# Kernel tuning notes

Measured on AMD Instinct MI355X. Metric: run time of the kernel, lower is better.

The kernel has to match this reference:

```python
import jax, jax.numpy as jnp
import numpy as np

L0, L1, L2 = 32, 16, 8
NS, NB = 512, 256
CUT = 7.0
N, E, G = 16384, 131072, 16
FEAT = L0 + 3 * L1 + 5 * L2  # 120


def setup_inputs() -> dict:
    key = jax.random.key(0)
    ks = jax.random.split(key, 16)
    rn = lambda k, s, sc=1.0: jax.random.normal(k, s, jnp.float32) * sc
    inp = {}
    inp['nodes'] = rn(ks[0], (N, FEAT))
    inp['pos'] = rn(ks[1], (N, 3)) * 5.0
    inp['cell'] = rn(ks[2], (G, 3, 3))
    inp['edge_shift'] = rn(ks[3], (E, 3))
    # tensor-product path weights (e3nn FullyConnectedTensorProduct, uvw mode)
    inp['W0'] = rn(ks[4], (L0, L0, NS))
    inp['W1'] = rn(ks[5], (L1, L1, NS))
    inp['W2'] = rn(ks[6], (L2, L2, NS))
    inp['ln_g'] = jnp.ones((NS,), jnp.float32)
    inp['ln_b'] = jnp.zeros((NS,), jnp.float32)
    inp['df_w1'] = rn(ks[7], (NB, 1024), NB ** -0.5)
    inp['df_b1'] = jnp.zeros((1024,), jnp.float32)
    inp['df_w2'] = rn(ks[8], (1024, NS), 1024 ** -0.5)
    inp['df_b2'] = jnp.zeros((NS,), jnp.float32)
    inp['mi_w1'] = rn(ks[9], (NS, 1024), NS ** -0.5)
    inp['mi_b1'] = jnp.zeros((1024,), jnp.float32)
    inp['mi_w2'] = rn(ks[10], (1024, 1024), 1024 ** -0.5)
    inp['mi_b2'] = jnp.zeros((1024,), jnp.float32)
    inp['mo_w'] = rn(ks[11], (1024, 1), 1024 ** -0.5)
    inp['mo_b'] = jnp.zeros((1,), jnp.float32)
    inp['edge_index'] = jax.random.randint(ks[12], (2, E), 0, N)
    inp['batch_vec'] = jnp.sort(jax.random.randint(ks[13], (N,), 0, G))
    return inp


def _split_irreps(x):
    x0 = x[:, :L0]                                   # (E, L0) scalars 0e
    x1 = x[:, L0:L0 + 3 * L1].reshape(-1, L1, 3)      # (E, L1, 3) vectors 1o
    x2 = x[:, L0 + 3 * L1:].reshape(-1, L2, 5)        # (E, L2, 5) 2e
    return x0, x1, x2


def reference(nodes, pos, cell, edge_shift, W0, W1, W2, ln_g, ln_b,
              df_w1, df_b1, df_w2, df_b2, mi_w1, mi_b1, mi_w2, mi_b2,
              mo_w, mo_b, edge_index, batch_vec):
    src, dst = edge_index[0], edge_index[1]
    # periodic-image translation vector per edge
    bcell = cell[batch_vec[src]]                      # (E,3,3)
    tvec = jnp.einsum('ei,eij->ej', edge_shift, bcell)
    radvec = pos[dst] - pos[src] + tvec               # (E,3)
    dist = jnp.linalg.norm(radvec, axis=1, keepdims=True)  # (E,1)
    r = 1.0 / (dist + 1e-6)
    # Bessel radial embedding with cutoff CUT, NB basis functions
    n = jnp.arange(1, NB + 1, dtype=jnp.float32)
    emb = jnp.sqrt(2.0 / CUT) * jnp.sin(n * jnp.pi * r / CUT) / r  # (E,NB)
    distfilter = jax.nn.silu(emb @ df_w1 + df_b1) @ df_w2 + df_b2  # (E,NS)

    # symmetrized fully-connected tensor product -> 0e scalars
    # 0.5*(tp(xs,xd)+tp(xd,xs)) == contraction of euv with symmetrized W
    xs0, xs1, xs2 = _split_irreps(nodes[src])
    xd0, xd1, xd2 = _split_irreps(nodes[dst])
    fan = jnp.sqrt(jnp.float32(L0 * L0 + L1 * L1 + L2 * L2))  # element path norm
    sym = lambda W: 0.5 * (W + W.transpose(1, 0, 2))
    e0 = jnp.einsum('eu,ev->euv', xs0, xd0)
    mixed = jnp.einsum('euv,uvw->ew', e0, sym(W0)) / fan
    e1 = jnp.einsum('eui,evi->euv', xs1, xd1)
    mixed = mixed + jnp.einsum('euv,uvw->ew', e1, sym(W1)) / (fan * jnp.sqrt(3.0))
    e2 = jnp.einsum('eui,evi->euv', xs2, xd2)
    mixed = mixed + jnp.einsum('euv,uvw->ew', e2, sym(W2)) / (fan * jnp.sqrt(5.0))

    # LayerNorm over numscalars
    mu = jnp.mean(mixed, axis=-1, keepdims=True)
    var = jnp.mean((mixed - mu) ** 2, axis=-1, keepdims=True)
    mixednorm = (mixed - mu) * jax.lax.rsqrt(var + 1e-5) * ln_g + ln_b

    reg = mixednorm * distfilter
    h = jax.nn.silu(reg @ mi_w1 + mi_b1)
    h = jax.nn.silu(h @ mi_w2 + mi_b2)
    return h @ mo_w + mo_b  # (E,1)
```

## Files before the change

### kernel.cpp

```cpp
#include <hip/hip_runtime.h>

#define EE 131072
#define NNODE 16384
#define FEAT 120
#define NS 512
#define NB 256
#define KCAT 1344

typedef unsigned short u16;
typedef __bf16 bf16x8 __attribute__((ext_vector_type(8)));
typedef float f32x4 __attribute__((ext_vector_type(4)));
typedef float f32x16 __attribute__((ext_vector_type(16)));
typedef unsigned short ushort8 __attribute__((ext_vector_type(8)));

__device__ __forceinline__ float b2f(u16 u) {
  union { unsigned int i; float f; } x; x.i = ((unsigned int)u) << 16; return x.f;
}
__device__ __forceinline__ u16 f2b(float f) {
  union { float f; unsigned int i; } x; x.f = f;
  unsigned int lsb = (x.i >> 16) & 1u;
  x.i += 0x7fffu + lsb;
  return (u16)(x.i >> 16);
}
__device__ __forceinline__ u16 f2b_fast(float f) {
  __bf16 h = (__bf16)f;
  union { __bf16 h; u16 u; } x; x.h = h; return x.u;
}
__device__ __forceinline__ float rdany(const void* p, long i, int f32) {
  return f32 ? ((const float*)p)[i] : b2f(((const u16*)p)[i]);
}

__device__ __forceinline__ void gload16(const u16* g, u16* l) {
  __builtin_amdgcn_global_load_lds(
      (__attribute__((address_space(1))) void*)(u16*)g,
      (__attribute__((address_space(3))) void*)l, 16, 0, 0);
}

__global__ void detect_k(const u16* __restrict__ nodes, int* __restrict__ flag) {
  __shared__ int cnt;
  if (threadIdx.x == 0) cnt = 0;
  __syncthreads();
  u16 v = nodes[threadIdx.x];
  int e = (v >> 7) & 0xFF;
  if (e >= 0x48) atomicAdd(&cnt, 1);
  __syncthreads();
  if (threadIdx.x == 0) *flag = (cnt >= 16) ? 1 : 0;
}

__global__ __launch_bounds__(256) void convert_k(const void* __restrict__ src,
                                                 u16* __restrict__ dst, long n,
                                                 const int* __restrict__ flag) {
  long i = (long)blockIdx.x * 256 + threadIdx.x;
  if (i >= n) return;
  if (*flag)
    dst[i] = f2b(((const float*)src)[i]);
  else
    dst[i] = ((const u16*)src)[i];
}

__global__ __launch_bounds__(256) void transpose_k(const u16* __restrict__ in,
                                                   u16* __restrict__ out, int R, int C) {
  __shared__ u16 tile[32][33];
  int c0 = blockIdx.x * 32, r0 = blockIdx.y * 32;
  int tx = threadIdx.x & 31, ty = threadIdx.x >> 5;
  for (int i = 0; i < 32; i += 8) {
    int r = r0 + ty + i, c = c0 + tx;
    if (r < R && c < C) tile[ty + i][tx] = in[(long)r * C + c];
  }
  __syncthreads();
  for (int i = 0; i < 32; i += 8) {
    int r = r0 + tx, c = c0 + ty + i;
    if (r < R && c < C) out[(long)c * R + r] = tile[tx][ty + i];
  }
}

__global__ __launch_bounds__(256) void build_wcat(const u16* __restrict__ W0,
                                                  const u16* __restrict__ W1,
                                                  const u16* __restrict__ W2,
                                                  u16* __restrict__ wcT) {
  int idx = blockIdx.x * 256 + threadIdx.x;
  if (idx >= NS * KCAT) return;
  int w = idx / KCAT, k = idx - w * KCAT;
  const float fan = 36.66060556f;
  float val;
  if (k < 1024) {
    int u = k >> 5, v = k & 31;
    val = 0.5f * (b2f(W0[(u * 32 + v) * NS + w]) + b2f(W0[(v * 32 + u) * NS + w])) / fan;
  } else if (k < 1280) {
    int j = k - 1024;
    int u = j >> 4, v = j & 15;
    val = 0.5f * (b2f(W1[(u * 16 + v) * NS + w]) + b2f(W1[(v * 16 + u) * NS + w])) /
          (fan * 1.7320508076f);
  } else {
    int j = k - 1280;
    int u = j >> 3, v = j & 7;
    val = 0.5f * (b2f(W2[(u * 8 + v) * NS + w]) + b2f(W2[(v * 8 + u) * NS + w])) /
          (fan * 2.2360679775f);
  }
  wcT[idx] = f2b(val);
}

__global__ __launch_bounds__(256) void edge_prep(
    const u16* __restrict__ nodes, const void* __restrict__ pos, const void* __restrict__ cell,
    const void* __restrict__ shift, const int* __restrict__ eidx, const int* __restrict__ batch,
    u16* __restrict__ emb, u16* __restrict__ ocat, int e0, const int* __restrict__ flag) {
  const int wave = threadIdx.x >> 6, lane = threadIdx.x & 63;
  const int el = blockIdx.x * 4 + wave;
  const int e = e0 + el;
  const int f32 = *flag;
  __shared__ u16 sxs[4][FEAT], sxd[4][FEAT];
  const int src = eidx[e], dst = eidx[EE + e];
  for (int i = lane; i < FEAT; i += 64) {
    sxs[wave][i] = nodes[(long)src * FEAT + i];
    sxd[wave][i] = nodes[(long)dst * FEAT + i];
  }
  __syncthreads();
  const int b = batch[src];
  float s0 = rdany(shift, (long)e * 3, f32), s1 = rdany(shift, (long)e * 3 + 1, f32),
        s2 = rdany(shift, (long)e * 3 + 2, f32);
  float d2 = 0.f;
#pragma unroll
  for (int j = 0; j < 3; j++) {
    float tv = s0 * rdany(cell, b * 9 + j, f32) + s1 * rdany(cell, b * 9 + 3 + j, f32) +
               s2 * rdany(cell, b * 9 + 6 + j, f32);
    float rv = rdany(pos, dst * 3 + j, f32) - rdany(pos, src * 3 + j, f32) + tv;
    d2 += rv * rv;
  }
  float dist = sqrtf(d2);
  float r = 1.0f / (dist + 1e-6f);
  const float c0 = 0.5345224838f;
  const float pi7 = 0.44879895051f;
#pragma unroll
  for (int j = 0; j < 4; j++) {
    int n = lane + 64 * j;
    float val = c0 * sinf((float)(n + 1) * pi7 * r) / r;
    emb[(long)el * NB + n] = f2b(val);
  }
  const u16* xs = sxs[wave];
  const u16* xd = sxd[wave];
  u16* orow = ocat + (long)el * KCAT;
#pragma unroll
  for (int j = 0; j < 16; j++) {
    int k = lane + 64 * j;
    int u = k >> 5, v = k & 31;
    orow[k] = f2b(b2f(xs[u]) * b2f(xd[v]));
  }
#pragma unroll
  for (int j = 0; j < 4; j++) {
    int k = lane + 64 * j;
    int u = k >> 4, v = k & 15;
    float s = 0.f;
#pragma unroll
    for (int i = 0; i < 3; i++) s += b2f(xs[32 + u * 3 + i]) * b2f(xd[32 + v * 3 + i]);
    orow[1024 + k] = f2b(s);
  }
  {
    int u = lane >> 3, v = lane & 7;
    float s = 0.f;
#pragma unroll
    for (int i = 0; i < 5; i++) s += b2f(xs[80 + u * 5 + i]) * b2f(xd[80 + v * 5 + i]);
    orow[1280 + lane] = f2b(s);
  }
}

#define STG_A(buf, h, kk)                                                        \
  do {                                                                           \
    gload16(Ag + ((h) * 128) * (long)K + (kk), &lA[buf][(h) * 8192 + tid * 8]);  \
    gload16(Ag + ((h) * 128 + 64) * (long)K + (kk),                              \
            &lA[buf][(h) * 8192 + 4096 + tid * 8]);                              \
  } while (0)
#define STG_B(buf, h, kk)                                                        \
  do {                                                                           \
    gload16(Bg + ((h) * 128) * (long)K + (kk), &lB[buf][(h) * 8192 + tid * 8]);  \
    gload16(Bg + ((h) * 128 + 64) * (long)K + (kk),                              \
            &lB[buf][(h) * 8192 + 4096 + tid * 8]);                              \
  } while (0)
#define RD_A(buf, fm, s)                                                         \
  (*(const bf16x8*)&lA[buf][((wm * 128 + (fm)*32 + l32) << 6) +                  \
                            ((((s)*2 + half) ^ r7) << 3)])
#define RD_B(buf, fn, s)                                                         \
  (*(const bf16x8*)&lB[buf][((wn * 64 + (fn)*32 + l32) << 6) +                   \
                            ((((s)*2 + half) ^ r7) << 3)])
#define MF(a, b, c) __builtin_amdgcn_mfma_f32_32x32x16_bf16(a, b, c, 0, 0, 0)

template <int ACT, int OF32, int HEAD>
__global__ __launch_bounds__(512, 2) void gemm_bt(const u16* __restrict__ A,
                                                  const u16* __restrict__ BT,
                                                  const u16* __restrict__ bias,
                                                  void* __restrict__ Cv,
                                                  const u16* __restrict__ hw,
                                                  float* __restrict__ outf, int N, int K) {
  __shared__ __align__(16) u16 lA[2][256 * 64];
  __shared__ __align__(16) u16 lB[2][256 * 64];
  const int tid = threadIdx.x;
  const int lane = tid & 63;
  const int wave = tid >> 6;
  const int half = lane >> 5, l32 = lane & 31, r7 = lane & 7;
  const int wm = wave >> 2, wn = wave & 3;

  const int nbn = N >> 8;
  int idx = blockIdx.x;
  if ((gridDim.x & 7) == 0) {
    int per = gridDim.x >> 3;
    idx = (blockIdx.x & 7) * per + (blockIdx.x >> 3);
  }
  const int mi = idx / nbn;
  const int ni = idx - mi * nbn;
  const long m0 = (long)mi * 256;
  const int n0 = ni << 8;
  const int nk = K >> 6;

  const int srow = tid >> 3;
  const int gseg = (tid & 7) ^ (srow & 7);
  const u16* Ag = A + (m0 + srow) * (long)K + gseg * 8;
  const u16* Bg = BT + (long)(n0 + srow) * K + gseg * 8;

  f32x16 acc[4][2];
#pragma unroll
  for (int i = 0; i < 4; i++)
#pragma unroll
    for (int j = 0; j < 2; j++)
#pragma unroll
      for (int q = 0; q < 16; q++) acc[i][j][q] = 0.f;

  STG_A(0, 0, 0);
  STG_A(0, 1, 0);
  STG_B(0, 0, 0);
  STG_B(0, 1, 0);
  if (nk > 1) {
    STG_B(1, 0, 64);
    STG_B(1, 1, 64);
    asm volatile("s_waitcnt vmcnt(4)" ::: "memory");
  } else {
    asm volatile("s_waitcnt vmcnt(0)" ::: "memory");
  }
  __builtin_amdgcn_s_barrier();

  bf16x8 av[2][4], b0[4], b1[4];

  for (int t = 0; t < nk; ++t) {
    const int cur = t & 1, nxt = cur ^ 1;
    const int kA = (t + 1) << 6;
    const int kB = (t + 2) << 6;
    const bool pA = (t + 1) < nk;
    const bool pB = (t + 2) < nk;

#pragma unroll
    for (int s = 0; s < 4; s++) {
      av[0][s] = RD_A(cur, 0, s);
      av[1][s] = RD_A(cur, 1, s);
      b0[s] = RD_B(cur, 0, s);
    }
    if (pA) STG_A(nxt, 0, kA);
    __builtin_amdgcn_s_barrier();
    asm volatile("s_waitcnt lgkmcnt(0)" ::: "memory");
    __builtin_amdgcn_s_setprio(1);
#pragma unroll
    for (int s = 0; s < 4; s++) {
      acc[0][0] = MF(av[0][s], b0[s], acc[0][0]);
      acc[1][0] = MF(av[1][s], b0[s], acc[1][0]);
    }
    __builtin_amdgcn_s_setprio(0);
    __builtin_amdgcn_s_barrier();

#pragma unroll
    for (int s = 0; s < 4; s++) b1[s] = RD_B(cur, 1, s);
    if (pA) STG_A(nxt, 1, kA);
    __builtin_amdgcn_s_barrier();
    asm volatile("s_waitcnt lgkmcnt(0)" ::: "memory");
    __builtin_amdgcn_s_setprio(1);
#pragma unroll
    for (int s = 0; s < 4; s++) {
      acc[0][1] = MF(av[0][s], b1[s], acc[0][1]);
      acc[1][1] = MF(av[1][s], b1[s], acc[1][1]);
    }
    __builtin_amdgcn_s_setprio(0);
    __builtin_amdgcn_s_barrier();

#pragma unroll
    for (int s = 0; s < 4; s++) {
      av[0][s] = RD_A(cur, 2, s);
      av[1][s] = RD_A(cur, 3, s);
    }
    if (pB) STG_B(cur, 0, kB);
    __builtin_amdgcn_s_barrier();
    asm volatile("s_waitcnt lgkmcnt(0)" ::: "memory");
    __builtin_amdgcn_s_setprio(1);
#pragma unroll
    for (int s = 0; s < 4; s++) {
      acc[2][0] = MF(av[0][s], b0[s], acc[2][0]);
      acc[3][0] = MF(av[1][s], b0[s], acc[3][0]);
    }
    __builtin_amdgcn_s_setprio(0);
    __builtin_amdgcn_s_barrier();

    if (pB) {
      STG_B(cur, 1, kB);
      asm volatile("s_waitcnt vmcnt(4)" ::: "memory");
    } else {
      asm volatile("s_waitcnt vmcnt(0)" ::: "memory");
    }
    __builtin_amdgcn_s_barrier();
    __builtin_amdgcn_s_setprio(1);
#pragma unroll
    for (int s = 0; s < 4; s++) {
      acc[2][1] = MF(av[0][s], b1[s], acc[2][1]);
      acc[3][1] = MF(av[1][s], b1[s], acc[3][1]);
    }
    __builtin_amdgcn_s_setprio(0);
    __builtin_amdgcn_s_barrier();
  }

  const int colb = n0 + wn * 64 + l32;
  float* Cf = (float*)Cv;
  u16* Cb = (u16*)Cv;
  if (HEAD) {
    const float bv0 = b2f(bias[colb]), bv1 = b2f(bias[colb + 32]);
    const float hw0 = b2f(hw[colb]), hw1 = b2f(hw[colb + 32]);
#pragma unroll
    for (int fm = 0; fm < 4; fm++) {
#pragma unroll
      for (int rg = 0; rg < 16; rg++) {
        float v0 = acc[fm][0][rg] + bv0;
        float v1 = acc[fm][1][rg] + bv1;
        if (ACT) {
          v0 = __fdividef(v0, 1.0f + __expf(-v0));
          v1 = __fdividef(v1, 1.0f + __expf(-v1));
        }
        float s = v0 * hw0 + v1 * hw1;
        s += __shfl_xor(s, 1);
        s += __shfl_xor(s, 2);
        s += __shfl_xor(s, 4);
        s += __shfl_xor(s, 8);
        s += __shfl_xor(s, 16);
        if (l32 == 0) {
          long row = m0 + wm * 128 + fm * 32 + (rg & 3) + ((rg >> 2) << 3) + (half << 2);
          atomicAdd(&outf[row], s);
        }
      }
    }
  } else {
    const float bv0 = bias ? b2f(bias[colb]) : 0.0f;
    const float bv1 = bias ? b2f(bias[colb + 32]) : 0.0f;
#pragma unroll
    for (int fm = 0; fm < 4; fm++) {
#pragma unroll
      for (int rg = 0; rg < 16; rg++) {
        long row = m0 + wm * 128 + fm * 32 + (rg & 3) + ((rg >> 2) << 3) + (half << 2);
        float v0 = acc[fm][0][rg] + bv0;
        float v1 = acc[fm][1][rg] + bv1;
        if (ACT) {
          v0 = __fdividef(v0, 1.0f + __expf(-v0));
          v1 = __fdividef(v1, 1.0f + __expf(-v1));
        }
        if (OF32) {
          Cf[row * N + colb] = v0;
          Cf[row * N + colb + 32] = v1;
        } else {
          Cb[row * N + colb] = f2b_fast(v0);
          Cb[row * N + colb + 32] = f2b_fast(v1);
        }
      }
    }
  }
}

__global__ __launch_bounds__(256) void ln_mul_k(const float* __restrict__ mixed,
                                                const u16* __restrict__ g,
                                                const u16* __restrict__ bvec,
                                                u16* __restrict__ dfreg) {
  const int wave = threadIdx.x >> 6, lane = threadIdx.x & 63;
  const long e = (long)blockIdx.x * 4 + wave;
  const float* row = mixed + e * NS;
  float x[8];
  f32x4 v0 = *(const f32x4*)&row[lane * 8];
  f32x4 v1 = *(const f32x4*)&row[lane * 8 + 4];
#pragma unroll
  for (int j = 0; j < 4; j++) { x[j] = v0[j]; x[4 + j] = v1[j]; }
  float s = 0.f, sq = 0.f;
#pragma unroll
  for (int j = 0; j < 8; j++) { s += x[j]; sq += x[j] * x[j]; }
  for (int o = 32; o; o >>= 1) { s += __shfl_xor(s, o); sq += __shfl_xor(sq, o); }
  float mu = s * (1.0f / 512.0f);
  float var = sq * (1.0f / 512.0f) - mu * mu;
  float rstd = rsqrtf(var + 1e-5f);
  u16* drow = dfreg + e * NS;
  ushort8 dv = *(const ushort8*)&drow[lane * 8];
  ushort8 ov;
#pragma unroll
  for (int j = 0; j < 8; j++) {
    int c = lane * 8 + j;
    float val = (x[j] - mu) * rstd * b2f(g[c]) + b2f(bvec[c]);
    ov[j] = f2b(val * b2f(dv[j]));
  }
  *(ushort8*)&drow[lane * 8] = ov;
}

__global__ __launch_bounds__(256) void head_finish(const float* __restrict__ outf,
                                                   const u16* __restrict__ b,
                                                   void* __restrict__ out,
                                                   const int* __restrict__ flag) {
  int e = blockIdx.x * 256 + threadIdx.x;
  float v = outf[e] + b2f(b[0]);
  if (*flag)
    ((float*)out)[e] = v;
  else
    ((u16*)out)[e] = f2b(v);
}

extern "C" void kernel_launch(void* const* d_in, const int* in_sizes, int n_in, void* d_out,
                              int out_size, void* d_ws, size_t ws_size, hipStream_t stream) {
  const int* eidx = (const int*)d_in[19];
  const int* batch = (const int*)d_in[20];

  char* ws = (char*)d_ws;
  size_t off = 0;
  auto alloc = [&](size_t bytes) {
    char* p = ws + off;
    off += (bytes + 255) & ~(size_t)255;
    return p;
  };

  int* flag = (int*)alloc(256);
  float* outf = (float*)alloc((size_t)EE * 4);

  detect_k<<<1, 256, 0, stream>>>((const u16*)d_in[0], flag);

  u16* cv[19];
  for (int i = 0; i < 19; i++) {
    long n = in_sizes[i];
    cv[i] = (u16*)alloc((size_t)n * 2);
    convert_k<<<(int)((n + 255) / 256), 256, 0, stream>>>(d_in[i], cv[i], n, flag);
  }
  const u16* nodes = cv[0];
  const u16* W0 = cv[4];
  const u16* W1 = cv[5];
  const u16* W2 = cv[6];
  const u16* ln_g = cv[7];
  const u16* ln_b = cv[8];
  const u16* df_w1 = cv[9];
  const u16* df_b1 = cv[10];
  const u16* df_w2 = cv[11];
  const u16* df_b2 = cv[12];
  const u16* mi_w1 = cv[13];
  const u16* mi_b1 = cv[14];
  const u16* mi_w2 = cv[15];
  const u16* mi_b2 = cv[16];
  const u16* mo_w = cv[17];
  const u16* mo_b = cv[18];

  u16* w1T = (u16*)alloc(1024 * 256 * 2);
  u16* w2T = (u16*)alloc(512 * 1024 * 2);
  u16* m1T = (u16*)alloc(1024 * 512 * 2);
  u16* m2T = (u16*)alloc((size_t)1024 * 1024 * 2);
  u16* wcT = (u16*)alloc((size_t)NS * KCAT * 2);

  int nchunk = 1;
  while (nchunk < 64) {
    size_t CHs = (size_t)(EE / nchunk);
    size_t need = off + CHs * 6272 + 8192;
    if (need <= ws_size) break;
    nchunk <<= 1;
  }
  const int CH = EE / nchunk;

  u16* ocat = (u16*)alloc((size_t)CH * KCAT * 2);
  u16* emb = (u16*)alloc((size_t)CH * NB * 2);
  u16* h1 = (u16*)alloc((size_t)CH * 1024 * 2);
  u16* dfb = (u16*)alloc((size_t)CH * NS * 2);
  u16* h2 = ocat;
  float* mixed = (float*)h1;

  transpose_k<<<dim3(1024 / 32, 256 / 32), 256, 0, stream>>>(df_w1, w1T, 256, 1024);
  transpose_k<<<dim3(512 / 32, 1024 / 32), 256, 0, stream>>>(df_w2, w2T, 1024, 512);
  transpose_k<<<dim3(1024 / 32, 512 / 32), 256, 0, stream>>>(mi_w1, m1T, 512, 1024);
  transpose_k<<<dim3(1024 / 32, 1024 / 32), 256, 0, stream>>>(mi_w2, m2T, 1024, 1024);
  build_wcat<<<(NS * KCAT + 255) / 256, 256, 0, stream>>>(W0, W1, W2, wcT);

  hipMemsetAsync(outf, 0, (size_t)EE * 4, stream);

  const int RB = CH / 256;
  for (int c = 0; c < nchunk; c++) {
    const int eb = c * CH;
    edge_prep<<<CH / 4, 256, 0, stream>>>(nodes, d_in[1], d_in[2], d_in[3], eidx, batch, emb,
                                          ocat, eb, flag);

    gemm_bt<1, 0, 0><<<RB * 4, 512, 0, stream>>>(emb, w1T, df_b1, h1, nullptr, nullptr, 1024, 256);
    gemm_bt<0, 0, 0><<<RB * 2, 512, 0, stream>>>(h1, w2T, df_b2, dfb, nullptr, nullptr, 512, 1024);

    gemm_bt<0, 1, 0><<<RB * 2, 512, 0, stream>>>(ocat, wcT, nullptr, mixed, nullptr, nullptr, 512,
                                                 1344);

    ln_mul_k<<<CH / 4, 256, 0, stream>>>(mixed, ln_g, ln_b, dfb);

    gemm_bt<1, 0, 0><<<RB * 4, 512, 0, stream>>>(dfb, m1T, mi_b1, h2, nullptr, nullptr, 1024, 512);
    gemm_bt<1, 0, 1><<<RB * 4, 512, 0, stream>>>(h2, m2T, mi_b2, nullptr, mo_w, outf + eb, 1024,
                                                 1024);
  }
  head_finish<<<EE / 256, 256, 0, stream>>>(outf, mo_b, d_out, flag);
}
```

Measured before the change: 1.475 ms.

## Switch GEMM to 16x16x32 MFMA tiles with new LDS swizzle and prefetch schedule

Rewrites the bf16 GEMM inner loop to use 16x16x32 MFMA instructions instead of 32x32x16, with an 8x4 grid of 4-wide accumulators per wave. The LDS read addressing and global-load swizzle are changed to match the new fragment layout. The prefetch schedule is restructured so part of the next A tile is loaded earlier, and one barrier per iteration is removed. Epilogues are rewritten for the new output layout. This may change MFMA throughput and LDS bank-conflict behaviour, and the new swizzle could introduce conflicts or correctness risk.

```diff
diff --git a/kernel.cpp b/kernel.cpp
--- a/kernel.cpp
+++ b/kernel.cpp
@@ -10,7 +10,6 @@
 typedef unsigned short u16;
 typedef __bf16 bf16x8 __attribute__((ext_vector_type(8)));
 typedef float f32x4 __attribute__((ext_vector_type(4)));
-typedef float f32x16 __attribute__((ext_vector_type(16)));
 typedef unsigned short ushort8 __attribute__((ext_vector_type(8)));
 
 __device__ __forceinline__ float b2f(u16 u) {
@@ -163,25 +162,27 @@
   }
 }
 
-#define STG_A(buf, h, kk)                                                        \
-  do {                                                                           \
-    gload16(Ag + ((h) * 128) * (long)K + (kk), &lA[buf][(h) * 8192 + tid * 8]);  \
-    gload16(Ag + ((h) * 128 + 64) * (long)K + (kk),                              \
-            &lA[buf][(h) * 8192 + 4096 + tid * 8]);                              \
+#define STGA(buf, h, part, kk)                                             \
+  gload16(Ag + ((h)*128 + (part)*64) * (long)K + (kk),                      \
+          &lA[buf][(h)*8192 + (part)*4096 + tid * 8])
+#define STGB(buf, h, part, kk)                                             \
+  gload16(Bg + ((h)*128 + (part)*64) * (long)K + (kk),                      \
+          &lB[buf][(h)*8192 + (part)*4096 + tid * 8])
+#define RDA(buf, fm, ks)                                                   \
+  (*(const bf16x8*)&lA[buf][((((wm * 128 + (fm)*16 + row_l) << 7) +        \
+                              (ks)*64 + kq16) >> 1)])
+#define RDB(buf, fn, ks)                                                   \
+  (*(const bf16x8*)&lB[buf][((((wn * 64 + (fn)*16 + row_l) << 7) +         \
+                              (ks)*64 + kq16) >> 1)])
+#define MF16(a, b, c) __builtin_amdgcn_mfma_f32_16x16x32_bf16(a, b, c, 0, 0, 0)
+#define MFQ(mh, nh)                                                        \
+  do {                                                                     \
+    _Pragma("unroll") for (int f = 0; f < 4; f++)                          \
+        _Pragma("unroll") for (int g = 0; g < 2; g++)                      \
+            _Pragma("unroll") for (int ks = 0; ks < 2; ks++)               \
+                acc[(mh)*4 + f][(nh)*2 + g] =                              \
+        MF16(af[f][ks], bf[(nh)*2 + g][ks], acc[(mh)*4 + f][(nh)*2 + g]);  \
   } while (0)
-#define STG_B(buf, h, kk)                                                        \
-  do {                                                                           \
-    gload16(Bg + ((h) * 128) * (long)K + (kk), &lB[buf][(h) * 8192 + tid * 8]);  \
-    gload16(Bg + ((h) * 128 + 64) * (long)K + (kk),                              \
-            &lB[buf][(h) * 8192 + 4096 + tid * 8]);                              \
-  } while (0)
-#define RD_A(buf, fm, s)                                                         \
-  (*(const bf16x8*)&lA[buf][((wm * 128 + (fm)*32 + l32) << 6) +                  \
-                            ((((s)*2 + half) ^ r7) << 3)])
-#define RD_B(buf, fn, s)                                                         \
-  (*(const bf16x8*)&lB[buf][((wn * 64 + (fn)*32 + l32) << 6) +                   \
-                            ((((s)*2 + half) ^ r7) << 3)])
-#define MF(a, b, c) __builtin_amdgcn_mfma_f32_32x32x16_bf16(a, b, c, 0, 0, 0)
 
 template <int ACT, int OF32, int HEAD>
 __global__ __launch_bounds__(512, 2) void gemm_bt(const u16* __restrict__ A,
@@ -190,13 +191,14 @@
                                                   void* __restrict__ Cv,
                                                   const u16* __restrict__ hw,
                                                   float* __restrict__ outf, int N, int K) {
-  __shared__ __align__(16) u16 lA[2][256 * 64];
-  __shared__ __align__(16) u16 lB[2][256 * 64];
+  __shared__ __align__(16) u16 lA[2][16384];
+  __shared__ __align__(16) u16 lB[2][16384];
   const int tid = threadIdx.x;
   const int lane = tid & 63;
   const int wave = tid >> 6;
-  const int half = lane >> 5, l32 = lane & 31, r7 = lane & 7;
   const int wm = wave >> 2, wn = wave & 3;
+  const int row_l = lane & 15;
+  const int kq16 = ((lane >> 4) * 16) ^ ((lane & 4) << 3);
 
   const int nbn = N >> 8;
   int idx = blockIdx.x;
@@ -211,154 +213,132 @@
   const int nk = K >> 6;
 
   const int srow = tid >> 3;
-  const int gseg = (tid & 7) ^ (srow & 7);
+  const int gseg = (tid & 7) ^ (((tid >> 5) & 1) << 1);
   const u16* Ag = A + (m0 + srow) * (long)K + gseg * 8;
   const u16* Bg = BT + (long)(n0 + srow) * K + gseg * 8;
 
-  f32x16 acc[4][2];
-#pragma unroll
-  for (int i = 0; i < 4; i++)
-#pragma unroll
-    for (int j = 0; j < 2; j++)
-#pragma unroll
-      for (int q = 0; q < 16; q++) acc[i][j][q] = 0.f;
-
-  STG_A(0, 0, 0);
-  STG_A(0, 1, 0);
-  STG_B(0, 0, 0);
-  STG_B(0, 1, 0);
+  f32x4 acc[8][4];
+#pragma unroll
+  for (int i = 0; i < 8; i++)
+#pragma unroll
+    for (int j = 0; j < 4; j++)
+#pragma unroll
+      for (int q = 0; q < 4; q++) acc[i][j][q] = 0.f;
+
+  STGA(0, 0, 0, 0); STGA(0, 0, 1, 0); STGA(0, 1, 0, 0); STGA(0, 1, 1, 0);
+  STGB(0, 0, 0, 0); STGB(0, 0, 1, 0); STGB(0, 1, 0, 0); STGB(0, 1, 1, 0);
   if (nk > 1) {
-    STG_B(1, 0, 64);
-    STG_B(1, 1, 64);
-    asm volatile("s_waitcnt vmcnt(4)" ::: "memory");
+    STGB(1, 0, 0, 64); STGB(1, 0, 1, 64); STGB(1, 1, 0, 64); STGB(1, 1, 1, 64);
+    STGA(1, 0, 0, 64); STGA(1, 0, 1, 64);
+    asm volatile("s_waitcnt vmcnt(6)" ::: "memory");
   } else {
     asm volatile("s_waitcnt vmcnt(0)" ::: "memory");
   }
   __builtin_amdgcn_s_barrier();
 
-  bf16x8 av[2][4], b0[4], b1[4];
+  bf16x8 af[4][2], bf[4][2];
 
   for (int t = 0; t < nk; ++t) {
     const int cur = t & 1, nxt = cur ^ 1;
-    const int kA = (t + 1) << 6;
-    const int kB = (t + 2) << 6;
+    const int kN = (t + 1) << 6;
+    const int kN2 = (t + 2) << 6;
     const bool pA = (t + 1) < nk;
-    const bool pB = (t + 2) < nk;
-
-#pragma unroll
-    for (int s = 0; s < 4; s++) {
-      av[0][s] = RD_A(cur, 0, s);
-      av[1][s] = RD_A(cur, 1, s);
-      b0[s] = RD_B(cur, 0, s);
-    }
-    if (pA) STG_A(nxt, 0, kA);
+    const bool p2 = (t + 2) < nk;
+
+#pragma unroll
+    for (int f = 0; f < 4; f++) { af[f][0] = RDA(cur, f, 0); af[f][1] = RDA(cur, f, 1); }
+#pragma unroll
+    for (int g = 0; g < 2; g++) { bf[g][0] = RDB(cur, g, 0); bf[g][1] = RDB(cur, g, 1); }
+    if (pA) { STGA(nxt, 1, 0, kN); STGA(nxt, 1, 1, kN); }
     __builtin_amdgcn_s_barrier();
     asm volatile("s_waitcnt lgkmcnt(0)" ::: "memory");
     __builtin_amdgcn_s_setprio(1);
-#pragma unroll
-    for (int s = 0; s < 4; s++) {
-      acc[0][0] = MF(av[0][s], b0[s], acc[0][0]);
-      acc[1][0] = MF(av[1][s], b0[s], acc[1][0]);
-    }
+    MFQ(0, 0);
     __builtin_amdgcn_s_setprio(0);
     __builtin_amdgcn_s_barrier();
 
 #pragma unroll
-    for (int s = 0; s < 4; s++) b1[s] = RD_B(cur, 1, s);
-    if (pA) STG_A(nxt, 1, kA);
+    for (int g = 0; g < 2; g++) { bf[2 + g][0] = RDB(cur, 2 + g, 0); bf[2 + g][1] = RDB(cur, 2 + g, 1); }
     __builtin_amdgcn_s_barrier();
     asm volatile("s_waitcnt lgkmcnt(0)" ::: "memory");
     __builtin_amdgcn_s_setprio(1);
-#pragma unroll
-    for (int s = 0; s < 4; s++) {
-      acc[0][1] = MF(av[0][s], b1[s], acc[0][1]);
-      acc[1][1] = MF(av[1][s], b1[s], acc[1][1]);
-    }
+    MFQ(0, 1);
     __builtin_amdgcn_s_setprio(0);
     __builtin_amdgcn_s_barrier();
 
 #pragma unroll
-    for (int s = 0; s < 4; s++) {
-      av[0][s] = RD_A(cur, 2, s);
-      av[1][s] = RD_A(cur, 3, s);
-    }
-    if (pB) STG_B(cur, 0, kB);
+    for (int f = 0; f < 4; f++) { af[f][0] = RDA(cur, 4 + f, 0); af[f][1] = RDA(cur, 4 + f, 1); }
+    if (p2) { STGB(cur, 0, 0, kN2); STGB(cur, 0, 1, kN2); }
     __builtin_amdgcn_s_barrier();
     asm volatile("s_waitcnt lgkmcnt(0)" ::: "memory");
     __builtin_amdgcn_s_setprio(1);
-#pragma unroll
-    for (int s = 0; s < 4; s++) {
-      acc[2][0] = MF(av[0][s], b0[s], acc[2][0]);
-      acc[3][0] = MF(av[1][s], b0[s], acc[3][0]);
+    MFQ(1, 0);
+    __builtin_amdgcn_s_setprio(0);
+    __builtin_amdgcn_s_barrier();
+
+    if (p2) {
+      STGB(cur, 1, 0, kN2); STGB(cur, 1, 1, kN2);
+      STGA(cur, 0, 0, kN2); STGA(cur, 0, 1, kN2);
     }
+    __builtin_amdgcn_s_setprio(1);
+    MFQ(1, 1);
     __builtin_amdgcn_s_setprio(0);
-    __builtin_amdgcn_s_barrier();
-
-    if (pB) {
-      STG_B(cur, 1, kB);
-      asm volatile("s_waitcnt vmcnt(4)" ::: "memory");
-    } else {
+    if (p2)
+      asm volatile("s_waitcnt vmcnt(6)" ::: "memory");
+    else
       asm volatile("s_waitcnt vmcnt(0)" ::: "memory");
-    }
-    __builtin_amdgcn_s_barrier();
-    __builtin_amdgcn_s_setprio(1);
-#pragma unroll
-    for (int s = 0; s < 4; s++) {
-      acc[2][1] = MF(av[0][s], b1[s], acc[2][1]);
-      acc[3][1] = MF(av[1][s], b1[s], acc[3][1]);
-    }
-    __builtin_amdgcn_s_setprio(0);
-    __builtin_amdgcn_s_barrier();
-  }
-
-  const int colb = n0 + wn * 64 + l32;
+    __builtin_amdgcn_s_barrier();
+  }
+
+  const int rql = (lane >> 4) * 2;
+  const int cl = lane & 15;
   float* Cf = (float*)Cv;
   u16* Cb = (u16*)Cv;
   if (HEAD) {
-    const float bv0 = b2f(bias[colb]), bv1 = b2f(bias[colb + 32]);
-    const float hw0 = b2f(hw[colb]), hw1 = b2f(hw[colb + 32]);
-#pragma unroll
-    for (int fm = 0; fm < 4; fm++) {
-#pragma unroll
-      for (int rg = 0; rg < 16; rg++) {
-        float v0 = acc[fm][0][rg] + bv0;
-        float v1 = acc[fm][1][rg] + bv1;
-        if (ACT) {
-          v0 = __fdividef(v0, 1.0f + __expf(-v0));
-          v1 = __fdividef(v1, 1.0f + __expf(-v1));
+    float bv[4], hv[4];
+#pragma unroll
+    for (int g = 0; g < 4; g++) {
+      const int col = n0 + wn * 64 + g * 16 + cl;
+      bv[g] = b2f(bias[col]);
+      hv[g] = b2f(hw[col]);
+    }
+#pragma unroll
+    for (int fm = 0; fm < 8; fm++) {
+#pragma unroll
+      for (int q = 0; q < 4; q++) {
+        float s = 0.f;
+#pragma unroll
+        for (int g = 0; g < 4; g++) {
+          float v = acc[fm][g][q] + bv[g];
+          if (ACT) v = __fdividef(v, 1.0f + __expf(-v));
+          s += v * hv[g];
         }
-        float s = v0 * hw0 + v1 * hw1;
         s += __shfl_xor(s, 1);
         s += __shfl_xor(s, 2);
         s += __shfl_xor(s, 4);
         s += __shfl_xor(s, 8);
-        s += __shfl_xor(s, 16);
-        if (l32 == 0) {
-          long row = m0 + wm * 128 + fm * 32 + (rg & 3) + ((rg >> 2) << 3) + (half << 2);
+        if (cl == 0) {
+          long row = m0 + wm * 128 + fm * 16 + rql * 2 + q;
           atomicAdd(&outf[row], s);
         }
       }
     }
   } else {
-    const float bv0 = bias ? b2f(bias[colb]) : 0.0f;
-    const float bv1 = bias ? b2f(bias[colb + 32]) : 0.0f;
-#pragma unroll
-    for (int fm = 0; fm < 4; fm++) {
-#pragma unroll
-      for (int rg = 0; rg < 16; rg++) {
-        long row = m0 + wm * 128 + fm * 32 + (rg & 3) + ((rg >> 2) << 3) + (half << 2);
-        float v0 = acc[fm][0][rg] + bv0;
-        float v1 = acc[fm][1][rg] + bv1;
-        if (ACT) {
-          v0 = __fdividef(v0, 1.0f + __expf(-v0));
-          v1 = __fdividef(v1, 1.0f + __expf(-v1));
-        }
-        if (OF32) {
-          Cf[row * N + colb] = v0;
-          Cf[row * N + colb + 32] = v1;
-        } else {
-          Cb[row * N + colb] = f2b_fast(v0);
-          Cb[row * N + colb + 32] = f2b_fast(v1);
+#pragma unroll
+    for (int fm = 0; fm < 8; fm++) {
+#pragma unroll
+      for (int g = 0; g < 4; g++) {
+        const int col = n0 + wn * 64 + g * 16 + cl;
+        const float bvv = bias ? b2f(bias[col]) : 0.0f;
+#pragma unroll
+        for (int q = 0; q < 4; q++) {
+          long row = m0 + wm * 128 + fm * 16 + rql * 2 + q;
+          float v = acc[fm][g][q] + bvv;
+          if (ACT) v = __fdividef(v, 1.0f + __expf(-v));
+          if (OF32)
+            Cf[row * N + col] = v;
+          else
+            Cb[row * N + col] = f2b_fast(v);
         }
       }
     }
```

Result: slower. 1.509 ms (+2.3%).
